# Kernel optimization log

Measured on AMD Instinct MI355X. Metric: run time of the kernel, lower is better.

## Reference

```python
import jax, jax.numpy as jnp
import numpy as np
from jax import lax

DM, DS, K, EXPAND = 512, 16, 4, 1
DI = EXPAND * DM           # d_inner
DT_RANK = (DM + 15) // 16  # ceil(d_model/16) = 32
B, L = 4, 2048


def setup_inputs() -> dict:
    key = jax.random.key(0)
    ks = jax.random.split(key, 10)
    x = jax.random.normal(ks[0], (B, L, DM), dtype=jnp.float32)
    W_in = jax.random.normal(ks[1], (2 * DI, DM), dtype=jnp.float32) * (1.0 / np.sqrt(DM))
    conv_w = jax.random.normal(ks[2], (DI, 1, K), dtype=jnp.float32) * (1.0 / np.sqrt(K))
    conv_b = jax.random.normal(ks[3], (DI,), dtype=jnp.float32) * 0.02
    W_xproj = jax.random.normal(ks[4], (DT_RANK + 2 * DS, DI), dtype=jnp.float32) * (1.0 / np.sqrt(DI))
    W_dt = jax.random.normal(ks[5], (DI, DT_RANK), dtype=jnp.float32) * (1.0 / np.sqrt(DT_RANK))
    b_dt = jax.random.uniform(ks[6], (DI,), dtype=jnp.float32, minval=-4.0, maxval=-2.0)  # softplus(b)~small dt
    A_log = jnp.log(jnp.broadcast_to(jnp.arange(1, DS + 1, dtype=jnp.float32), (DI, DS)))
    D_param = jnp.ones((DI,), dtype=jnp.float32)
    W_out = jax.random.normal(ks[7], (DM, DI), dtype=jnp.float32) * (1.0 / np.sqrt(DI))
    return {"x": x, "W_in": W_in, "conv_w": conv_w, "conv_b": conv_b,
            "W_xproj": W_xproj, "W_dt": W_dt, "b_dt": b_dt,
            "A_log": A_log, "D_param": D_param, "W_out": W_out}


def _mamba(x, W_in, conv_w, conv_b, W_xproj, W_dt, b_dt, A_log, D_param, W_out):
    # in_proj -> x, z branches [B,L,DI] each
    xz = jnp.einsum('bld,ed->ble', x, W_in)
    xc, z = xz[..., :DI], xz[..., DI:]
    # causal depthwise conv1d over time
    xt = jnp.transpose(xc, (0, 2, 1))                      # [B,DI,L]
    xt = jnp.pad(xt, ((0, 0), (0, 0), (K - 1, 0)))
    xt = lax.conv_general_dilated(xt, conv_w, (1,), 'VALID',
                                  dimension_numbers=('NCH', 'OIH', 'NCH'),
                                  feature_group_count=DI)
    xt = xt + conv_b[None, :, None]
    xc = jax.nn.silu(jnp.transpose(xt, (0, 2, 1)))         # [B,L,DI]
    # input-dependent dt, B, C
    x_dbl = jnp.einsum('bld,ed->ble', xc, W_xproj)         # [B,L,DT_RANK+2*DS]
    dt = x_dbl[..., :DT_RANK]
    Bm = x_dbl[..., DT_RANK:DT_RANK + DS]                  # [B,L,DS]
    Cm = x_dbl[..., DT_RANK + DS:]                         # [B,L,DS]
    dt = jax.nn.softplus(jnp.einsum('blr,dr->bld', dt, W_dt) + b_dt)  # [B,L,DI]
    A = -jnp.exp(A_log)                                    # [DI,DS]
    deltaA = jnp.exp(dt[..., None] * A)                    # [B,L,DI,DS]
    deltaBu = dt[..., None] * Bm[:, :, None, :] * xc[..., None]       # [B,L,DI,DS]

    def step(h, inp):
        dA_t, dBu_t, C_t = inp                             # [B,DI,DS],[B,DI,DS],[B,DS]
        h = dA_t * h + dBu_t
        y = jnp.einsum('bds,bs->bd', h, C_t)
        return h, y

    h0 = jnp.zeros((x.shape[0], DI, DS), dtype=x.dtype)
    _, ys = lax.scan(step, h0, (jnp.transpose(deltaA, (1, 0, 2, 3)),
                                jnp.transpose(deltaBu, (1, 0, 2, 3)),
                                jnp.transpose(Cm, (1, 0, 2))))
    y = jnp.transpose(ys, (1, 0, 2)) + xc * D_param        # [B,L,DI]
    y = y * jax.nn.silu(z)
    out = jnp.einsum('bld,ed->ble', y, W_out)              # [B,L,DM]
    out = jnp.clip(out, -1000.0, 1000.0)
    out = jnp.nan_to_num(out, nan=0.0, posinf=1000.0, neginf=-1000.0)
    return out


def reference(x, W_in, conv_w, conv_b, W_xproj, W_dt, b_dt, A_log, D_param, W_out):
    return _mamba(x, W_in, conv_w, conv_b, W_xproj, W_dt, b_dt, A_log, D_param, W_out)
```

## Files before the change

### kernel.cpp

```cpp
#include <hip/hip_runtime.h>
#include <math.h>

#define DMc   512
#define DIc   512
#define DSc   16
#define KCc   4
#define DTRc  32
#define NXDc  64
#define LLEN  2048
#define BBc   4
#define BLT   (BBc*LLEN)

#define NCH   128
#define CLEN  (LLEN/NCH)

typedef __attribute__((ext_vector_type(8))) short short8;
typedef __attribute__((ext_vector_type(8))) unsigned short ushort8;
typedef __attribute__((ext_vector_type(4))) float f32x4;

__device__ __forceinline__ float sigmoidf_(float x) { return 1.f / (1.f + __expf(-x)); }

__device__ __forceinline__ unsigned short f2bf(float x) {
    unsigned int u = __float_as_uint(x);
    u = (u + 0x7FFFu + ((u >> 16) & 1u)) >> 16;
    return (unsigned short)u;
}

#define CN1 (BLT * DMc / 8)
#define CN2 (1024 * DMc / 8)
#define CN3 (DMc * DIc / 8)
__global__ __launch_bounds__(256) void convert3_kernel(const float* __restrict__ x,
                                                       const float* __restrict__ Win,
                                                       const float* __restrict__ Wout,
                                                       unsigned short* __restrict__ xb,
                                                       unsigned short* __restrict__ Wb,
                                                       unsigned short* __restrict__ Wob)
{
    int i = blockIdx.x * 256 + threadIdx.x;
    const float* src; unsigned short* dst;
    if (i < CN1)                  { src = x;    dst = xb;  }
    else if (i < CN1 + CN2)       { src = Win;  dst = Wb;  i -= CN1; }
    else if (i < CN1 + CN2 + CN3) { src = Wout; dst = Wob; i -= CN1 + CN2; }
    else return;
    float4 a = ((const float4*)src)[2 * i];
    float4 b = ((const float4*)src)[2 * i + 1];
    ushort8 o;
    o[0] = f2bf(a.x); o[1] = f2bf(a.y); o[2] = f2bf(a.z); o[3] = f2bf(a.w);
    o[4] = f2bf(b.x); o[5] = f2bf(b.y); o[6] = f2bf(b.z); o[7] = f2bf(b.w);
    ((ushort8*)dst)[i] = o;
}

__global__ __launch_bounds__(256) void gemm_bt_f32(const float* __restrict__ A,
                                                   const float* __restrict__ Bw,
                                                   float* __restrict__ C,
                                                   int M, int N, int Kd,
                                                   int lda, int ldb)
{
    __shared__ float As[16][68];
    __shared__ float Bs[16][68];
    const int tid  = threadIdx.x;
    const int tx   = tid & 15;
    const int ty   = tid >> 4;
    const int arow = tid >> 2;
    const int akq  = (tid & 3) << 2;

    const float* Ab = A  + (size_t)(blockIdx.y * 64 + arow) * lda + akq;
    const float* Bb = Bw + (size_t)(blockIdx.x * 64 + arow) * ldb + akq;

    float acc[4][4] = {};

    for (int k0 = 0; k0 < Kd; k0 += 16) {
        float4 av = *(const float4*)(Ab + k0);
        float4 bv = *(const float4*)(Bb + k0);
        __syncthreads();
        As[akq + 0][arow] = av.x; As[akq + 1][arow] = av.y;
        As[akq + 2][arow] = av.z; As[akq + 3][arow] = av.w;
        Bs[akq + 0][arow] = bv.x; Bs[akq + 1][arow] = bv.y;
        Bs[akq + 2][arow] = bv.z; Bs[akq + 3][arow] = bv.w;
        __syncthreads();
#pragma unroll
        for (int k = 0; k < 16; ++k) {
            float4 a = *(const float4*)&As[k][ty << 2];
            float4 b = *(const float4*)&Bs[k][tx << 2];
            float ar[4] = {a.x, a.y, a.z, a.w};
            float br[4] = {b.x, b.y, b.z, b.w};
#pragma unroll
            for (int i = 0; i < 4; ++i)
#pragma unroll
                for (int j = 0; j < 4; ++j)
                    acc[i][j] += ar[i] * br[j];
        }
    }

#pragma unroll
    for (int i = 0; i < 4; ++i) {
        float4 v = make_float4(acc[i][0], acc[i][1], acc[i][2], acc[i][3]);
        *(float4*)(C + (size_t)(blockIdx.y * 64 + (ty << 2) + i) * N
                     + blockIdx.x * 64 + (tx << 2)) = v;
    }
}

template<int EPI>
__global__ __launch_bounds__(256) void gemm_mfma(const unsigned short* __restrict__ A,
                                                 const unsigned short* __restrict__ Bw,
                                                 float* __restrict__ C,
                                                 int M, int N, int Kd)
{
    __shared__ short As[128][40];
    __shared__ short Bs[128][40];
    const int tid  = threadIdx.x;
    const int lane = tid & 63;
    const int wv   = tid >> 6;
    const int wr   = wv >> 1;
    const int wc   = wv & 1;
    const int fr   = lane & 15;
    const int fq   = lane >> 4;

    const int rowA0 = blockIdx.y * 128;
    const int rowB0 = blockIdx.x * 128;

    const int r0 = tid >> 2,        s0 = (tid & 3) << 3;
    const int r1 = (tid + 256) >> 2, s1 = s0;

    f32x4 acc[4][4];
#pragma unroll
    for (int m = 0; m < 4; ++m)
#pragma unroll
        for (int n = 0; n < 4; ++n) acc[m][n] = (f32x4){0.f, 0.f, 0.f, 0.f};

    for (int k0 = 0; k0 < Kd; k0 += 32) {
        short8 a0 = *(const short8*)(A  + (size_t)(rowA0 + r0) * Kd + k0 + s0);
        short8 a1 = *(const short8*)(A  + (size_t)(rowA0 + r1) * Kd + k0 + s1);
        short8 b0 = *(const short8*)(Bw + (size_t)(rowB0 + r0) * Kd + k0 + s0);
        short8 b1 = *(const short8*)(Bw + (size_t)(rowB0 + r1) * Kd + k0 + s1);
        __syncthreads();
        *(short8*)&As[r0][s0] = a0;
        *(short8*)&As[r1][s1] = a1;
        *(short8*)&Bs[r0][s0] = b0;
        *(short8*)&Bs[r1][s1] = b1;
        __syncthreads();

        short8 af[4], bf[4];
#pragma unroll
        for (int m = 0; m < 4; ++m)
            af[m] = *(const short8*)&As[wr * 64 + m * 16 + fr][fq << 3];
#pragma unroll
        for (int n = 0; n < 4; ++n)
            bf[n] = *(const short8*)&Bs[wc * 64 + n * 16 + fr][fq << 3];
#pragma unroll
        for (int m = 0; m < 4; ++m)
#pragma unroll
            for (int n = 0; n < 4; ++n)
                acc[m][n] = __builtin_amdgcn_mfma_f32_16x16x32_bf16(af[m], bf[n], acc[m][n], 0, 0, 0);
    }

    const int crow0 = rowA0 + wr * 64 + (fq << 2);
    const int ccol0 = rowB0 + wc * 64 + fr;
#pragma unroll
    for (int m = 0; m < 4; ++m)
#pragma unroll
        for (int n = 0; n < 4; ++n)
#pragma unroll
            for (int j = 0; j < 4; ++j) {
                float v = acc[m][n][j];
                if (EPI) v = (v != v) ? 0.f : fminf(fmaxf(v, -1000.f), 1000.f);
                C[(size_t)(crow0 + m * 16 + j) * N + ccol0 + n * 16] = v;
            }
}

__global__ __launch_bounds__(256) void conv_silu_kernel(const float* __restrict__ xz,
                                                        const float* __restrict__ cw,
                                                        const float* __restrict__ cb,
                                                        float* __restrict__ xc)
{
    int gid = blockIdx.x * 256 + threadIdx.x;
    int d = gid & (DIc - 1);
    int l = (gid >> 9) & (LLEN - 1);
    int b = gid >> 20;
    float s = cb[d];
#pragma unroll
    for (int k = 0; k < KCc; ++k) {
        int ls = l + k - (KCc - 1);
        if (ls >= 0)
            s += xz[((size_t)(b * LLEN + ls) << 10) + d] * cw[d * KCc + k];
    }
    xc[gid] = s * sigmoidf_(s);
}

__device__ __forceinline__ size_t hs_off(int b, int c, int s, int d) {
    return ((size_t)((b * NCH + c) * DSc + s) << 9) + d;
}

__global__ __launch_bounds__(256) void scan_phase1(const float* __restrict__ xc,
                                                   const float* __restrict__ xdbl,
                                                   const float* __restrict__ Wdt,
                                                   const float* __restrict__ bdt,
                                                   const float* __restrict__ A_log,
                                                   float* __restrict__ hstate,
                                                   float* __restrict__ sdtbuf)
{
    int half = blockIdx.x & 1;
    int c    = (blockIdx.x >> 1) & (NCH - 1);
    int b    = blockIdx.x >> 8;
    int d    = (half << 8) + threadIdx.x;

    float A[DSc];
#pragma unroll
    for (int s = 0; s < DSc; ++s) A[s] = -__expf(A_log[d * DSc + s]);
    float wdt[DTRc];
#pragma unroll
    for (int i = 0; i < DTRc; ++i) wdt[i] = Wdt[d * DTRc + i];
    float bd = bdt[d];

    float h[DSc];
#pragma unroll
    for (int s = 0; s < DSc; ++s) h[s] = 0.f;
    float Sdt = 0.f;

    int row0 = b * LLEN + c * CLEN;
    for (int t = 0; t < CLEN; ++t) {
        int row = row0 + t;
        const float* xd = xdbl + (size_t)row * NXDc;
        float sdot = bd;
#pragma unroll
        for (int i = 0; i < DTRc; ++i) sdot += xd[i] * wdt[i];
        float dtv = fmaxf(sdot, 0.f) + log1pf(__expf(-fabsf(sdot)));
        float xcv = xc[((size_t)row << 9) + d];
        Sdt += dtv;
        float dBx = dtv * xcv;
#pragma unroll
        for (int s = 0; s < DSc; ++s)
            h[s] = __expf(dtv * A[s]) * h[s] + dBx * xd[DTRc + s];
    }
#pragma unroll
    for (int s = 0; s < DSc; ++s) hstate[hs_off(b, c, s, d)] = h[s];
    sdtbuf[((size_t)(b * NCH + c) << 9) + d] = Sdt;
}

__global__ __launch_bounds__(64) void scan_phase2(float* __restrict__ hstate,
                                                  const float* __restrict__ sdtbuf,
                                                  const float* __restrict__ A_log)
{
    int gid = blockIdx.x * 64 + threadIdx.x;
    int d = gid & (DIc - 1);
    int s = (gid >> 9) & (DSc - 1);
    int b = gid >> 13;

    float A = -__expf(A_log[d * DSc + s]);
    float h = 0.f;
    for (int c = 0; c < NCH; ++c) {
        size_t o = hs_off(b, c, s, d);
        float he  = hstate[o];
        float Sdt = sdtbuf[((size_t)(b * NCH + c) << 9) + d];
        hstate[o] = h;
        h = __expf(A * Sdt) * h + he;
    }
}

__global__ __launch_bounds__(256) void scan_phase3(const float* __restrict__ xc,
                                                   const float* __restrict__ xdbl,
                                                   const float* __restrict__ Wdt,
                                                   const float* __restrict__ bdt,
                                                   const float* __restrict__ xzbuf,
                                                   const float* __restrict__ hstate,
                                                   const float* __restrict__ A_log,
                                                   const float* __restrict__ Dp,
                                                   unsigned short* __restrict__ yb)
{
    int half = blockIdx.x & 1;
    int c    = (blockIdx.x >> 1) & (NCH - 1);
    int b    = blockIdx.x >> 8;
    int d    = (half << 8) + threadIdx.x;

    float A[DSc];
#pragma unroll
    for (int s = 0; s < DSc; ++s) A[s] = -__expf(A_log[d * DSc + s]);
    float wdt[DTRc];
#pragma unroll
    for (int i = 0; i < DTRc; ++i) wdt[i] = Wdt[d * DTRc + i];
    float bd = bdt[d];
    float Dv = Dp[d];

    float h[DSc];
#pragma unroll
    for (int s = 0; s < DSc; ++s) h[s] = hstate[hs_off(b, c, s, d)];

    int row0 = b * LLEN + c * CLEN;
    for (int t = 0; t < CLEN; ++t) {
        int row = row0 + t;
        const float* xd = xdbl + (size_t)row * NXDc;
        float sdot = bd;
#pragma unroll
        for (int i = 0; i < DTRc; ++i) sdot += xd[i] * wdt[i];
        float dtv = fmaxf(sdot, 0.f) + log1pf(__expf(-fabsf(sdot)));
        float xcv = xc[((size_t)row << 9) + d];
        float zv  = xzbuf[((size_t)row << 10) + DIc + d];
        float dBx = dtv * xcv;
        float acc = 0.f;
#pragma unroll
        for (int s = 0; s < DSc; ++s) {
            float dA = __expf(dtv * A[s]);
            h[s] = dA * h[s] + dBx * xd[DTRc + s];
            acc += h[s] * xd[DTRc + DSc + s];
        }
        float yv = (acc + xcv * Dv) * (zv * sigmoidf_(zv));
        yb[((size_t)row << 9) + d] = f2bf(yv);
    }
}

extern "C" void kernel_launch(void* const* d_in, const int* in_sizes, int n_in,
                              void* d_out, int out_size, void* d_ws, size_t ws_size,
                              hipStream_t stream)
{
    const float* x      = (const float*)d_in[0];
    const float* W_in   = (const float*)d_in[1];
    const float* conv_w = (const float*)d_in[2];
    const float* conv_b = (const float*)d_in[3];
    const float* W_xp   = (const float*)d_in[4];
    const float* W_dt   = (const float*)d_in[5];
    const float* b_dt   = (const float*)d_in[6];
    const float* A_log  = (const float*)d_in[7];
    const float* D_par  = (const float*)d_in[8];
    const float* W_out  = (const float*)d_in[9];
    float* out = (float*)d_out;

    float* ws   = (float*)d_ws;
    float* xz   = ws;
    float* xc   = xz + (size_t)BLT * 1024;
    float* xdbl = xc + (size_t)BLT * DIc;
    unsigned short* xb  = (unsigned short*)(xdbl + (size_t)BLT * NXDc);
    unsigned short* Wb  = xb + (size_t)BLT * DIc;
    unsigned short* Wob = Wb + (size_t)1024 * DMc;
    float* hstate = (float*)(Wob + (size_t)DMc * DIc);
    float* sdtbuf = hstate + (size_t)BBc * NCH * DSc * DIc;

    convert3_kernel<<<(CN1 + CN2 + CN3 + 255) / 256, 256, 0, stream>>>(
        x, W_in, W_out, xb, Wb, Wob);

    gemm_mfma<0><<<dim3(1024 / 128, BLT / 128), 256, 0, stream>>>(xb, Wb, xz, BLT, 1024, DMc);

    conv_silu_kernel<<<(BLT * DIc) / 256, 256, 0, stream>>>(xz, conv_w, conv_b, xc);

    gemm_bt_f32<<<dim3(1, BLT / 64), 256, 0, stream>>>(xc, W_xp, xdbl,
                                                       BLT, NXDc, DIc, DIc, DIc);

    scan_phase1<<<BBc * NCH * 2, 256, 0, stream>>>(xc, xdbl, W_dt, b_dt, A_log,
                                                   hstate, sdtbuf);
    scan_phase2<<<(BBc * DSc * DIc) / 64, 64, 0, stream>>>(hstate, sdtbuf, A_log);
    scan_phase3<<<BBc * NCH * 2, 256, 0, stream>>>(xc, xdbl, W_dt, b_dt, xz,
                                                   hstate, A_log, D_par, xb);

    gemm_mfma<1><<<dim3(DMc / 128, BLT / 128), 256, 0, stream>>>(xb, Wob, out, BLT, DMc, DMc);
}
```

Before: 181.6 us.

## Precompute dt via GEMM with softplus epilogue and stage B/C in LDS for scans

The dt projection and softplus are taken out of both scan phases and computed once by a small fp32 GEMM. Its bias-plus-softplus epilogue writes dt into the now-free x half of the xz buffer. The scan kernels preload per-chunk dt, xc and z values into registers and stage the B/C rows in shared memory, then run a fully unrolled time loop. This removes a 32-wide dot product per timestep that was repeated in phase 1 and phase 3, at the cost of an extra kernel launch, a round trip of dt through memory, and higher register pressure from the 16-element preload arrays.

```diff
diff --git a/kernel.cpp b/kernel.cpp
--- a/kernel.cpp
+++ b/kernel.cpp
@@ -50,11 +50,13 @@
     ((ushort8*)dst)[i] = o;
 }
 
+template<int EPI>
 __global__ __launch_bounds__(256) void gemm_bt_f32(const float* __restrict__ A,
                                                    const float* __restrict__ Bw,
+                                                   const float* __restrict__ bias,
                                                    float* __restrict__ C,
                                                    int M, int N, int Kd,
-                                                   int lda, int ldb)
+                                                   int lda, int ldb, int ldc)
 {
     __shared__ float As[16][68];
     __shared__ float Bs[16][68];
@@ -92,11 +94,21 @@
         }
     }
 
+    float4 bv = make_float4(0.f, 0.f, 0.f, 0.f);
+    if (EPI == 2) bv = *(const float4*)(bias + blockIdx.x * 64 + (tx << 2));
 #pragma unroll
     for (int i = 0; i < 4; ++i) {
-        float4 v = make_float4(acc[i][0], acc[i][1], acc[i][2], acc[i][3]);
-        *(float4*)(C + (size_t)(blockIdx.y * 64 + (ty << 2) + i) * N
-                     + blockIdx.x * 64 + (tx << 2)) = v;
+        float v[4] = {acc[i][0], acc[i][1], acc[i][2], acc[i][3]};
+        if (EPI == 2) {
+            float bb[4] = {bv.x, bv.y, bv.z, bv.w};
+#pragma unroll
+            for (int j = 0; j < 4; ++j) {
+                float s = v[j] + bb[j];
+                v[j] = fmaxf(s, 0.f) + log1pf(__expf(-fabsf(s)));
+            }
+        }
+        *(float4*)(C + (size_t)(blockIdx.y * 64 + (ty << 2) + i) * ldc
+                     + blockIdx.x * 64 + (tx << 2)) = make_float4(v[0], v[1], v[2], v[3]);
     }
 }
 
@@ -191,10 +203,9 @@
     return ((size_t)((b * NCH + c) * DSc + s) << 9) + d;
 }
 
-__global__ __launch_bounds__(256) void scan_phase1(const float* __restrict__ xc,
+__global__ __launch_bounds__(256) void scan_phase1(const float* __restrict__ dtz,
+                                                   const float* __restrict__ xc,
                                                    const float* __restrict__ xdbl,
-                                                   const float* __restrict__ Wdt,
-                                                   const float* __restrict__ bdt,
                                                    const float* __restrict__ A_log,
                                                    float* __restrict__ hstate,
                                                    float* __restrict__ sdtbuf)
@@ -203,34 +214,36 @@
     int c    = (blockIdx.x >> 1) & (NCH - 1);
     int b    = blockIdx.x >> 8;
     int d    = (half << 8) + threadIdx.x;
+    int row0 = b * LLEN + c * CLEN;
+
+    __shared__ float bc[CLEN][32];
+    {
+        int r = threadIdx.x >> 4, col = (threadIdx.x & 15) << 1;
+        const float* src = xdbl + (size_t)(row0 + r) * NXDc + DTRc + col;
+        bc[r][col] = src[0]; bc[r][col + 1] = src[1];
+    }
 
     float A[DSc];
 #pragma unroll
     for (int s = 0; s < DSc; ++s) A[s] = -__expf(A_log[d * DSc + s]);
-    float wdt[DTRc];
-#pragma unroll
-    for (int i = 0; i < DTRc; ++i) wdt[i] = Wdt[d * DTRc + i];
-    float bd = bdt[d];
-
-    float h[DSc];
-#pragma unroll
-    for (int s = 0; s < DSc; ++s) h[s] = 0.f;
+
+    float dtv[CLEN], xcv[CLEN];
+#pragma unroll
+    for (int t = 0; t < CLEN; ++t) {
+        dtv[t] = dtz[((size_t)(row0 + t) << 10) + d];
+        xcv[t] = xc [((size_t)(row0 + t) << 9) + d];
+    }
+    __syncthreads();
+
+    float h[DSc] = {};
     float Sdt = 0.f;
-
-    int row0 = b * LLEN + c * CLEN;
+#pragma unroll
     for (int t = 0; t < CLEN; ++t) {
-        int row = row0 + t;
-        const float* xd = xdbl + (size_t)row * NXDc;
-        float sdot = bd;
-#pragma unroll
-        for (int i = 0; i < DTRc; ++i) sdot += xd[i] * wdt[i];
-        float dtv = fmaxf(sdot, 0.f) + log1pf(__expf(-fabsf(sdot)));
-        float xcv = xc[((size_t)row << 9) + d];
-        Sdt += dtv;
-        float dBx = dtv * xcv;
+        float dBx = dtv[t] * xcv[t];
+        Sdt += dtv[t];
 #pragma unroll
         for (int s = 0; s < DSc; ++s)
-            h[s] = __expf(dtv * A[s]) * h[s] + dBx * xd[DTRc + s];
+            h[s] = __expf(dtv[t] * A[s]) * h[s] + dBx * bc[t][s];
     }
 #pragma unroll
     for (int s = 0; s < DSc; ++s) hstate[hs_off(b, c, s, d)] = h[s];
@@ -257,11 +270,9 @@
     }
 }
 
-__global__ __launch_bounds__(256) void scan_phase3(const float* __restrict__ xc,
+__global__ __launch_bounds__(256) void scan_phase3(const float* __restrict__ dtz,
+                                                   const float* __restrict__ xc,
                                                    const float* __restrict__ xdbl,
-                                                   const float* __restrict__ Wdt,
-                                                   const float* __restrict__ bdt,
-                                                   const float* __restrict__ xzbuf,
                                                    const float* __restrict__ hstate,
                                                    const float* __restrict__ A_log,
                                                    const float* __restrict__ Dp,
@@ -271,40 +282,45 @@
     int c    = (blockIdx.x >> 1) & (NCH - 1);
     int b    = blockIdx.x >> 8;
     int d    = (half << 8) + threadIdx.x;
+    int row0 = b * LLEN + c * CLEN;
+
+    __shared__ float bc[CLEN][32];
+    {
+        int r = threadIdx.x >> 4, col = (threadIdx.x & 15) << 1;
+        const float* src = xdbl + (size_t)(row0 + r) * NXDc + DTRc + col;
+        bc[r][col] = src[0]; bc[r][col + 1] = src[1];
+    }
 
     float A[DSc];
 #pragma unroll
     for (int s = 0; s < DSc; ++s) A[s] = -__expf(A_log[d * DSc + s]);
-    float wdt[DTRc];
-#pragma unroll
-    for (int i = 0; i < DTRc; ++i) wdt[i] = Wdt[d * DTRc + i];
-    float bd = bdt[d];
     float Dv = Dp[d];
 
+    float dtv[CLEN], xcv[CLEN], zv[CLEN];
+#pragma unroll
+    for (int t = 0; t < CLEN; ++t) {
+        dtv[t] = dtz[((size_t)(row0 + t) << 10) + d];
+        xcv[t] = xc [((size_t)(row0 + t) << 9) + d];
+        zv[t]  = dtz[((size_t)(row0 + t) << 10) + DIc + d];
+    }
+
     float h[DSc];
 #pragma unroll
     for (int s = 0; s < DSc; ++s) h[s] = hstate[hs_off(b, c, s, d)];
-
-    int row0 = b * LLEN + c * CLEN;
+    __syncthreads();
+
+#pragma unroll
     for (int t = 0; t < CLEN; ++t) {
-        int row = row0 + t;
-        const float* xd = xdbl + (size_t)row * NXDc;
-        float sdot = bd;
-#pragma unroll
-        for (int i = 0; i < DTRc; ++i) sdot += xd[i] * wdt[i];
-        float dtv = fmaxf(sdot, 0.f) + log1pf(__expf(-fabsf(sdot)));
-        float xcv = xc[((size_t)row << 9) + d];
-        float zv  = xzbuf[((size_t)row << 10) + DIc + d];
-        float dBx = dtv * xcv;
+        float dBx = dtv[t] * xcv[t];
         float acc = 0.f;
 #pragma unroll
         for (int s = 0; s < DSc; ++s) {
-            float dA = __expf(dtv * A[s]);
-            h[s] = dA * h[s] + dBx * xd[DTRc + s];
-            acc += h[s] * xd[DTRc + DSc + s];
+            float dA = __expf(dtv[t] * A[s]);
+            h[s] = dA * h[s] + dBx * bc[t][s];
+            acc += h[s] * bc[t][DSc + s];
         }
-        float yv = (acc + xcv * Dv) * (zv * sigmoidf_(zv));
-        yb[((size_t)row << 9) + d] = f2bf(yv);
+        float yv = (acc + xcv[t] * Dv) * (zv[t] * sigmoidf_(zv[t]));
+        yb[((size_t)(row0 + t) << 9) + d] = f2bf(yv);
     }
 }
 
@@ -341,14 +357,15 @@
 
     conv_silu_kernel<<<(BLT * DIc) / 256, 256, 0, stream>>>(xz, conv_w, conv_b, xc);
 
-    gemm_bt_f32<<<dim3(1, BLT / 64), 256, 0, stream>>>(xc, W_xp, xdbl,
-                                                       BLT, NXDc, DIc, DIc, DIc);
-
-    scan_phase1<<<BBc * NCH * 2, 256, 0, stream>>>(xc, xdbl, W_dt, b_dt, A_log,
-                                                   hstate, sdtbuf);
+    gemm_bt_f32<0><<<dim3(1, BLT / 64), 256, 0, stream>>>(xc, W_xp, nullptr, xdbl,
+                                                          BLT, NXDc, DIc, DIc, DIc, NXDc);
+
+    gemm_bt_f32<2><<<dim3(DIc / 64, BLT / 64), 256, 0, stream>>>(xdbl, W_dt, b_dt, xz,
+                                                                 BLT, DIc, DTRc, NXDc, DTRc, 1024);
+
+    scan_phase1<<<BBc * NCH * 2, 256, 0, stream>>>(xz, xc, xdbl, A_log, hstate, sdtbuf);
     scan_phase2<<<(BBc * DSc * DIc) / 64, 64, 0, stream>>>(hstate, sdtbuf, A_log);
-    scan_phase3<<<BBc * NCH * 2, 256, 0, stream>>>(xc, xdbl, W_dt, b_dt, xz,
-                                                   hstate, A_log, D_par, xb);
+    scan_phase3<<<BBc * NCH * 2, 256, 0, stream>>>(xz, xc, xdbl, hstate, A_log, D_par, xb);
 
     gemm_mfma<1><<<dim3(DMc / 128, BLT / 128), 256, 0, stream>>>(xb, Wob, out, BLT, DMc, DMc);
 }
```

Result: faster. 169.6 us (-6.6%).
